# Kernel optimization log

Hardware: AMD Instinct MI355X
Metric: run time of the kernel (lower is better)

Reference implementation:

```python
import jax, jax.numpy as jnp
import numpy as np

KEY_DIM = 1024
SCALE = KEY_DIM ** -0.5


def setup_inputs() -> dict:
    key = jax.random.key(0)
    k1, k2, k3, k4 = jax.random.split(key, 4)
    B, S, E = 4, 2048, 1024
    x = jax.random.normal(k1, (B, S, E), dtype=jnp.float32)
    WQ = jax.random.normal(k2, (KEY_DIM, E), dtype=jnp.float32) * (E ** -0.5)
    WK = jax.random.normal(k3, (KEY_DIM, E), dtype=jnp.float32) * (E ** -0.5)
    WV = jax.random.normal(k4, (KEY_DIM, E), dtype=jnp.float32) * (E ** -0.5)
    return {"x": x, "WQ": WQ, "WK": WK, "WV": WV}


def reference(x, WQ, WK, WV):
    # x: [B, S, E]; Linear(bias=False) weights are [out, in] as in torch.
    q = jnp.einsum('bse,ke->bsk', x, WQ)   # [B, S, K]
    k = jnp.einsum('bse,ke->bsk', x, WK)   # [B, S, K]
    v = jnp.einsum('bse,ve->bsv', x, WV)   # [B, S, V]
    scores = jnp.einsum('bsk,btk->bst', q, k) * SCALE  # [B, S, S]
    # Faithful to torch: mask where tril(scores) == 0 (upper triangle).
    masked = jnp.where(jnp.tril(scores) == 0, -jnp.inf, scores)
    attn = jax.nn.softmax(masked, axis=-1)
    return jnp.einsum('bst,btv->bsv', attn, v)  # dropout=0.0 -> identity
```

## Files before the change

### kernel.cpp

```cpp
#include <hip/hip_runtime.h>

typedef _Float16 f16x8 __attribute__((ext_vector_type(8)));
typedef unsigned short u16x8v __attribute__((ext_vector_type(8)));
typedef unsigned short u16x4v __attribute__((ext_vector_type(4)));
typedef float f32x4 __attribute__((ext_vector_type(4)));

constexpr int SEQ = 2048;
constexpr int DIM = 1024;
constexpr int BATCH = 4;
constexpr size_t NBS = (size_t)BATCH * SEQ * DIM;

static __device__ __forceinline__ unsigned short f2h(float f) {
    return __builtin_bit_cast(unsigned short, (_Float16)f);
}
static __device__ __forceinline__ float h2f(unsigned short u) {
    return (float)__builtin_bit_cast(_Float16, u);
}
static __device__ __forceinline__ f16x8 ldsld(const unsigned short* p) {
    return __builtin_bit_cast(f16x8, *(const u16x8v*)p);
}
static __device__ __forceinline__ void gld_lds16(const unsigned short* g, unsigned short* l) {
    __builtin_amdgcn_global_load_lds(
        (const __attribute__((address_space(1))) void*)g,
        (__attribute__((address_space(3))) void*)l, 16, 0, 0);
}

__global__ __launch_bounds__(256) void cvt_all(
    const float* __restrict__ X,
    const float* __restrict__ W0, const float* __restrict__ W1,
    const float* __restrict__ W2,
    unsigned short* __restrict__ Xf, unsigned short* __restrict__ Wf)
{
    const int b = blockIdx.x;
    const float* src;
    unsigned short* dst;
    int i;
    if (b < 8192) {
        src = X; dst = Xf;
        i = b * 256 + threadIdx.x;
    } else {
        const int wb = b - 8192;
        const int z = wb >> 10;
        src = (z == 0) ? W0 : (z == 1) ? W1 : W2;
        dst = Wf + (size_t)z * DIM * DIM;
        i = (wb & 1023) * 256 + threadIdx.x;
    }
    float4 f = ((const float4*)src)[i];
    u16x4v h;
    h.x = f2h(f.x); h.y = f2h(f.y); h.z = f2h(f.z); h.w = f2h(f.w);
    ((u16x4v*)dst)[i] = h;
}

__global__ __launch_bounds__(256) void mt_gemm(
    const unsigned short* __restrict__ Wqf, const unsigned short* __restrict__ Wkf,
    unsigned short* __restrict__ Mt)
{
    __shared__ __attribute__((aligned(16))) unsigned short As[64 * 128];
    __shared__ __attribute__((aligned(16))) unsigned short Bs[64 * 128];
    const int e0p = blockIdx.x * 128;
    const int e0  = blockIdx.y * 128;
    const int tid = threadIdx.x;
    const int w = tid >> 6, lane = tid & 63, q = lane >> 4, c = lane & 15;
    const int wrow = (w >> 1) * 64, wcol = (w & 1) * 64;
    const int kr = lane >> 4;
    const int un = lane & 15;

    f32x4 acc[4][4];
#pragma unroll
    for (int a = 0; a < 4; ++a)
#pragma unroll
        for (int b = 0; b < 4; ++b) acc[a][b] = (f32x4){0.f, 0.f, 0.f, 0.f};

    for (int k0 = 0; k0 < DIM; k0 += 64) {
        __syncthreads();
#pragma unroll
        for (int j = 0; j < 4; ++j) {
            const size_t ga = (size_t)(k0 + w * 16 + j * 4 + kr) * DIM;
            unsigned short* la = As + (w * 16 + j * 4) * 128;
            unsigned short* lb = Bs + (w * 16 + j * 4) * 128;
            gld_lds16(Wkf + ga + e0p + un * 8, la);
            gld_lds16(Wqf + ga + e0  + un * 8, lb);
        }
        __syncthreads();
#pragma unroll
        for (int kk = 0; kk < 2; ++kk) {
            f16x8 af[4], bf[4];
#pragma unroll
            for (int mi = 0; mi < 4; ++mi) {
                u16x8v t_;
#pragma unroll
                for (int j = 0; j < 8; ++j)
                    t_[j] = As[(kk * 32 + q * 8 + j) * 128 + wrow + mi * 16 + c];
                af[mi] = __builtin_bit_cast(f16x8, t_);
            }
#pragma unroll
            for (int ni = 0; ni < 4; ++ni) {
                u16x8v t_;
#pragma unroll
                for (int j = 0; j < 8; ++j)
                    t_[j] = Bs[(kk * 32 + q * 8 + j) * 128 + wcol + ni * 16 + c];
                bf[ni] = __builtin_bit_cast(f16x8, t_);
            }
#pragma unroll
            for (int mi = 0; mi < 4; ++mi)
#pragma unroll
                for (int ni = 0; ni < 4; ++ni)
                    acc[mi][ni] = __builtin_amdgcn_mfma_f32_16x16x32_f16(af[mi], bf[ni], acc[mi][ni], 0, 0, 0);
        }
    }
#pragma unroll
    for (int mi = 0; mi < 4; ++mi)
#pragma unroll
        for (int ni = 0; ni < 4; ++ni) {
            const int col = e0 + wcol + ni * 16 + c;
#pragma unroll
            for (int r = 0; r < 4; ++r) {
                const int row = e0p + wrow + mi * 16 + q * 4 + r;
                Mt[(size_t)row * DIM + col] = f2h(acc[mi][ni][r]);
            }
        }
}

__global__ __launch_bounds__(256) void yv_gemm(
    const unsigned short* __restrict__ Xf, const unsigned short* __restrict__ Mt,
    const unsigned short* __restrict__ Wvf,
    unsigned short* __restrict__ Yf, unsigned short* __restrict__ Vt)
{
    __shared__ __attribute__((aligned(16))) unsigned short Ah[128 * 64];
    __shared__ __attribute__((aligned(16))) unsigned short Bh[128 * 64];
    const int m0 = blockIdx.x * 128, n0 = blockIdx.y * 128, z = blockIdx.z;
    const unsigned short* Wz = z ? Wvf : Mt;
    const int tid = threadIdx.x;
    const int w = tid >> 6, lane = tid & 63, q = lane >> 4, c = lane & 15;
    const int wrow = (w >> 1) * 64, wcol = (w & 1) * 64;
    const int g8 = lane >> 3;
    const int cu = (lane & 7) ^ g8;
    const int srow = w * 8 + g8;
    const int scol = cu * 8;
    unsigned short* lA = Ah + w * 512;
    unsigned short* lB = Bh + w * 512;
    const int c7 = c & 7;

    f32x4 acc[4][4];
#pragma unroll
    for (int a = 0; a < 4; ++a)
#pragma unroll
        for (int b = 0; b < 4; ++b) acc[a][b] = (f32x4){0.f, 0.f, 0.f, 0.f};

    for (int k0 = 0; k0 < DIM; k0 += 64) {
        __syncthreads();
        {
            const size_t ga = (size_t)(m0 + srow) * DIM + k0 + scol;
            const size_t gb = (size_t)(n0 + srow) * DIM + k0 + scol;
#pragma unroll
            for (int j = 0; j < 4; ++j) {
                gld_lds16(Xf + ga + (size_t)(j * 32) * DIM, lA + j * 2048);
                gld_lds16(Wz + gb + (size_t)(j * 32) * DIM, lB + j * 2048);
            }
        }
        __syncthreads();
#pragma unroll
        for (int kk = 0; kk < 2; ++kk) {
            f16x8 ah[4], bh[4];
#pragma unroll
            for (int mi = 0; mi < 4; ++mi)
                ah[mi] = ldsld(Ah + (wrow + mi * 16 + c) * 64 + (((kk << 2) + q) ^ c7) * 8);
#pragma unroll
            for (int ni = 0; ni < 4; ++ni)
                bh[ni] = ldsld(Bh + (wcol + ni * 16 + c) * 64 + (((kk << 2) + q) ^ c7) * 8);
#pragma unroll
            for (int mi = 0; mi < 4; ++mi)
#pragma unroll
                for (int ni = 0; ni < 4; ++ni)
                    acc[mi][ni] = __builtin_amdgcn_mfma_f32_16x16x32_f16(ah[mi], bh[ni], acc[mi][ni], 0, 0, 0);
        }
    }

    if (z == 1) {
#pragma unroll
        for (int mi = 0; mi < 4; ++mi) {
            const int mg = m0 + wrow + mi * 16 + q * 4;
            const int bb = mg >> 11, ss = mg & (SEQ - 1);
#pragma unroll
            for (int ni = 0; ni < 4; ++ni) {
                const int col = n0 + wcol + ni * 16 + c;
                u16x4v v;
                v.x = f2h(acc[mi][ni][0]);
                v.y = f2h(acc[mi][ni][1]);
                v.z = f2h(acc[mi][ni][2]);
                v.w = f2h(acc[mi][ni][3]);
                *(u16x4v*)(Vt + ((size_t)bb * DIM + col) * SEQ + ss) = v;
            }
        }
    } else {
#pragma unroll
        for (int mi = 0; mi < 4; ++mi)
#pragma unroll
            for (int ni = 0; ni < 4; ++ni) {
                const int col = n0 + wcol + ni * 16 + c;
#pragma unroll
                for (int r = 0; r < 4; ++r) {
                    const int row = m0 + wrow + mi * 16 + q * 4 + r;
                    Yf[(size_t)row * DIM + col] = f2h(acc[mi][ni][r]);
                }
            }
    }
}

__global__ __launch_bounds__(256) void scores_gemm1b(
    const unsigned short* __restrict__ Q, const unsigned short* __restrict__ K,
    unsigned short* __restrict__ S)
{
    __shared__ __attribute__((aligned(16))) unsigned short Ah[128 * 64];
    __shared__ __attribute__((aligned(16))) unsigned short Bh[128 * 64];
    const int t = blockIdx.x;
    int ti = (int)((__builtin_sqrtf(8.f * t + 1.f) - 1.f) * 0.5f);
    while ((ti + 1) * (ti + 2) / 2 <= t) ++ti;
    while (ti * (ti + 1) / 2 > t) --ti;
    const int tj = t - ti * (ti + 1) / 2;
    const int i0 = ti * 128, j0 = tj * 128, b = blockIdx.z;
    const unsigned short* Qb = Q + (size_t)b * SEQ * DIM;
    const unsigned short* Kb = K + (size_t)b * SEQ * DIM;
    unsigned short* Sb = S + (size_t)b * SEQ * SEQ;
    const int tid = threadIdx.x;
    const int w = tid >> 6, lane = tid & 63, q = lane >> 4, c = lane & 15;
    const int wrow = (w >> 1) * 64, wcol = (w & 1) * 64;
    const int g8 = lane >> 3;
    const int cu = (lane & 7) ^ g8;
    const int srow = w * 8 + g8;
    const int scol = cu * 8;
    unsigned short* lA = Ah + w * 512;
    unsigned short* lB = Bh + w * 512;
    const int c7 = c & 7;

    f32x4 acc[4][4];
#pragma unroll
    for (int a = 0; a < 4; ++a)
#pragma unroll
        for (int bq = 0; bq < 4; ++bq) acc[a][bq] = (f32x4){0.f, 0.f, 0.f, 0.f};

    for (int k0 = 0; k0 < DIM; k0 += 64) {
        __syncthreads();
        {
            const size_t ga = (size_t)(i0 + srow) * DIM + k0 + scol;
            const size_t gb = (size_t)(j0 + srow) * DIM + k0 + scol;
#pragma unroll
            for (int j = 0; j < 4; ++j) {
                gld_lds16(Qb + ga + (size_t)(j * 32) * DIM, lA + j * 2048);
                gld_lds16(Kb + gb + (size_t)(j * 32) * DIM, lB + j * 2048);
            }
        }
        __syncthreads();
#pragma unroll
        for (int kk = 0; kk < 2; ++kk) {
            f16x8 ah[4], bh[4];
#pragma unroll
            for (int mi = 0; mi < 4; ++mi)
                ah[mi] = ldsld(Ah + (wrow + mi * 16 + c) * 64 + (((kk << 2) + q) ^ c7) * 8);
#pragma unroll
            for (int ni = 0; ni < 4; ++ni)
                bh[ni] = ldsld(Bh + (wcol + ni * 16 + c) * 64 + (((kk << 2) + q) ^ c7) * 8);
#pragma unroll
            for (int mi = 0; mi < 4; ++mi)
#pragma unroll
                for (int ni = 0; ni < 4; ++ni)
                    acc[mi][ni] = __builtin_amdgcn_mfma_f32_16x16x32_f16(ah[mi], bh[ni], acc[mi][ni], 0, 0, 0);
        }
    }
#pragma unroll
    for (int mi = 0; mi < 4; ++mi)
#pragma unroll
        for (int ni = 0; ni < 4; ++ni) {
            const int col = j0 + wcol + ni * 16 + c;
#pragma unroll
            for (int r = 0; r < 4; ++r) {
                const int row = i0 + wrow + mi * 16 + q * 4 + r;
                const float sc = acc[mi][ni][r] * 0.03125f;
                Sb[(size_t)row * SEQ + col] =
                    (sc == 0.f) ? (unsigned short)0xFC00u : f2h(sc);
            }
        }
}

__global__ __launch_bounds__(256) void softmax_row_b(
    const unsigned short* __restrict__ S, unsigned short* __restrict__ P)
{
    const int i = blockIdx.x, t = threadIdx.x;
    const size_t ro = ((size_t)blockIdx.y * SEQ + i) * SEQ;
    const int wid = t >> 6, lane = t & 63;
    __shared__ float redm[4], reds[4];
    const int j0 = t * 8;
    const int rti = (i & ~127) + 128;
    float sv[8];
    float mx = -__builtin_inff();
    if (j0 <= i) {
        u16x8v raw = *(const u16x8v*)(S + ro + j0);
#pragma unroll
        for (int u = 0; u < 8; ++u) {
            float s = (j0 + u <= i) ? h2f(raw[u]) : -__builtin_inff();
            sv[u] = s;
            mx = fmaxf(mx, s);
        }
    } else {
#pragma unroll
        for (int u = 0; u < 8; ++u) sv[u] = -__builtin_inff();
    }
#pragma unroll
    for (int off = 1; off < 64; off <<= 1) mx = fmaxf(mx, __shfl_xor(mx, off));
    if (lane == 0) redm[wid] = mx;
    __syncthreads();
    const float M = fmaxf(fmaxf(redm[0], redm[1]), fmaxf(redm[2], redm[3]));
    float sum = 0.f;
#pragma unroll
    for (int u = 0; u < 8; ++u) {
        float e = __expf(sv[u] - M);
        sv[u] = e;
        sum += e;
    }
#pragma unroll
    for (int off = 1; off < 64; off <<= 1) sum += __shfl_xor(sum, off);
    if (lane == 0) reds[wid] = sum;
    __syncthreads();
    const float rinv = 1.f / (reds[0] + reds[1] + reds[2] + reds[3]);
    if (j0 < rti) {
        u16x8v o;
#pragma unroll
        for (int u = 0; u < 8; ++u) o[u] = f2h(sv[u] * rinv);
        *(u16x8v*)(P + ro + j0) = o;
    }
}

__global__ __launch_bounds__(256) void pv_gemm(
    const unsigned short* __restrict__ Pm, const unsigned short* __restrict__ Vt,
    float* __restrict__ Out)
{
    __shared__ __attribute__((aligned(16))) unsigned short Ps[128 * 64];
    __shared__ __attribute__((aligned(16))) unsigned short Vs[128 * 64];
    const int b = blockIdx.z;
    const int i0t = (b < 2) ? blockIdx.x : 15 - blockIdx.x;
    const int i0 = i0t * 128, d0 = blockIdx.y * 128;
    const int tid = threadIdx.x;
    const int w = tid >> 6, lane = tid & 63, q = lane >> 4, c = lane & 15;
    const int wrow = (w >> 1) * 64, wcol = (w & 1) * 64;
    const int g8 = lane >> 3;
    const int cu = (lane & 7) ^ g8;
    const int srow = w * 8 + g8;
    const int scol = cu * 8;
    unsigned short* lA = Ps + w * 512;
    unsigned short* lB = Vs + w * 512;
    const int c7 = c & 7;

    f32x4 acc[4][4];
#pragma unroll
    for (int a = 0; a < 4; ++a)
#pragma unroll
        for (int bq = 0; bq < 4; ++bq) acc[a][bq] = (f32x4){0.f, 0.f, 0.f, 0.f};

    const int njs = 2 * i0t + 2;

    for (int ks = 0; ks < njs; ++ks) {
        const int j0 = ks * 64;
        __syncthreads();
        {
            const size_t gpa = ((size_t)b * SEQ + i0 + srow) * SEQ + j0 + scol;
            const size_t gva = ((size_t)b * DIM + d0 + srow) * SEQ + j0 + scol;
#pragma unroll
            for (int j = 0; j < 4; ++j) {
                gld_lds16(Pm + gpa + (size_t)(j * 32) * SEQ, lA + j * 2048);
                gld_lds16(Vt + gva + (size_t)(j * 32) * SEQ, lB + j * 2048);
            }
        }
        __syncthreads();
#pragma unroll
        for (int kk = 0; kk < 2; ++kk) {
            f16x8 ah[4], bh[4];
#pragma unroll
            for (int mi = 0; mi < 4; ++mi)
                ah[mi] = ldsld(Ps + (wrow + mi * 16 + c) * 64 + (((kk << 2) + q) ^ c7) * 8);
#pragma unroll
            for (int ni = 0; ni < 4; ++ni)
                bh[ni] = ldsld(Vs + (wcol + ni * 16 + c) * 64 + (((kk << 2) + q) ^ c7) * 8);
#pragma unroll
            for (int mi = 0; mi < 4; ++mi)
#pragma unroll
                for (int ni = 0; ni < 4; ++ni)
                    acc[mi][ni] = __builtin_amdgcn_mfma_f32_16x16x32_f16(ah[mi], bh[ni], acc[mi][ni], 0, 0, 0);
        }
    }
#pragma unroll
    for (int mi = 0; mi < 4; ++mi)
#pragma unroll
        for (int ni = 0; ni < 4; ++ni) {
            const int dcol = d0 + wcol + ni * 16 + c;
#pragma unroll
            for (int r = 0; r < 4; ++r) {
                const int i = i0 + wrow + mi * 16 + q * 4 + r;
                Out[((size_t)b * SEQ + i) * DIM + dcol] = acc[mi][ni][r];
            }
        }
}

extern "C" void kernel_launch(void* const* d_in, const int* in_sizes, int n_in,
                              void* d_out, int out_size, void* d_ws, size_t ws_size,
                              hipStream_t stream)
{
    (void)out_size; (void)ws_size;
    const float* X = nullptr;
    const float* Wv[3] = {nullptr, nullptr, nullptr};
    int nw = 0;
    for (int i = 0; i < n_in; ++i) {
        if (in_sizes[i] == (int)NBS)
            X = (const float*)d_in[i];
        else if (nw < 3)
            Wv[nw++] = (const float*)d_in[i];
    }

    unsigned short* ws = (unsigned short*)d_ws;
    unsigned short* Yf = ws;
    unsigned short* Vt = ws + 2 * NBS;
    unsigned short* Xf = ws + 3 * NBS;
    unsigned short* Pp = ws + 3 * NBS;
    unsigned short* Sb = ws + 5 * NBS;
    unsigned short* Wf = ws + 7 * NBS;
    unsigned short* Mtb = Wf + (size_t)3 * DIM * DIM;
    float* Out = (float*)d_out;

    cvt_all<<<dim3(8192 + 3072), 256, 0, stream>>>(X, Wv[0], Wv[1], Wv[2], Xf, Wf);

    mt_gemm<<<dim3(8, 8), 256, 0, stream>>>(
        Wf, Wf + (size_t)DIM * DIM, Mtb);

    yv_gemm<<<dim3(64, 8, 2), 256, 0, stream>>>(
        Xf, Mtb, Wf + (size_t)2 * DIM * DIM, Yf, Vt);

    scores_gemm1b<<<dim3(136, 1, BATCH), 256, 0, stream>>>(Yf, Xf, Sb);
    softmax_row_b<<<dim3(SEQ, BATCH), 256, 0, stream>>>(Sb, Pp);

    pv_gemm<<<dim3(16, 8, BATCH), 256, 0, stream>>>(Pp, Vt, Out);
}
```

Baseline: 259.1 us.

## Pre-transpose WQ/WK in convert kernel, swizzle mt_gemm LDS, remap scores grid

```diff
diff --git a/kernel.cpp b/kernel.cpp
--- a/kernel.cpp
+++ b/kernel.cpp
@@ -29,78 +29,103 @@
     const float* __restrict__ X,
     const float* __restrict__ W0, const float* __restrict__ W1,
     const float* __restrict__ W2,
-    unsigned short* __restrict__ Xf, unsigned short* __restrict__ Wf)
-{
+    unsigned short* __restrict__ Xf, unsigned short* __restrict__ Wf,
+    unsigned short* __restrict__ WqT, unsigned short* __restrict__ WkT)
+{
+    __shared__ __attribute__((aligned(16))) unsigned short T[64][72];
     const int b = blockIdx.x;
-    const float* src;
-    unsigned short* dst;
-    int i;
-    if (b < 8192) {
-        src = X; dst = Xf;
-        i = b * 256 + threadIdx.x;
-    } else {
-        const int wb = b - 8192;
-        const int z = wb >> 10;
-        src = (z == 0) ? W0 : (z == 1) ? W1 : W2;
-        dst = Wf + (size_t)z * DIM * DIM;
-        i = (wb & 1023) * 256 + threadIdx.x;
-    }
-    float4 f = ((const float4*)src)[i];
-    u16x4v h;
-    h.x = f2h(f.x); h.y = f2h(f.y); h.z = f2h(f.z); h.w = f2h(f.w);
-    ((u16x4v*)dst)[i] = h;
+    const int t = threadIdx.x;
+    if (b < 11264) {
+        const float* src;
+        unsigned short* dst;
+        int i;
+        if (b < 8192) {
+            src = X; dst = Xf;
+            i = b * 256 + t;
+        } else {
+            const int wb = b - 8192;
+            const int z = wb >> 10;
+            src = (z == 0) ? W0 : (z == 1) ? W1 : W2;
+            dst = Wf + (size_t)z * DIM * DIM;
+            i = (wb & 1023) * 256 + t;
+        }
+        float4 f = ((const float4*)src)[i];
+        u16x4v h;
+        h.x = f2h(f.x); h.y = f2h(f.y); h.z = f2h(f.z); h.w = f2h(f.w);
+        ((u16x4v*)dst)[i] = h;
+        return;
+    }
+    const int tb = b - 11264;
+    const float* src = (tb < 256) ? W0 : W1;
+    unsigned short* dst = (tb < 256) ? WqT : WkT;
+    const int tile = tb & 255;
+    const int tk = (tile >> 4) * 64;
+    const int te = (tile & 15) * 64;
+    const int cu = t & 15, kr4 = t >> 4;
+#pragma unroll
+    for (int p = 0; p < 4; ++p) {
+        const int k = p * 16 + kr4;
+        float4 v = *(const float4*)(src + (size_t)(tk + k) * DIM + te + cu * 4);
+        T[cu * 4 + 0][k] = f2h(v.x);
+        T[cu * 4 + 1][k] = f2h(v.y);
+        T[cu * 4 + 2][k] = f2h(v.z);
+        T[cu * 4 + 3][k] = f2h(v.w);
+    }
+    __syncthreads();
+    const int un = t & 7, er = t >> 3;
+#pragma unroll
+    for (int p = 0; p < 2; ++p) {
+        const int e = p * 32 + er;
+        *(u16x8v*)(dst + (size_t)(te + e) * DIM + tk + un * 8) =
+            *(const u16x8v*)&T[e][un * 8];
+    }
 }
 
 __global__ __launch_bounds__(256) void mt_gemm(
-    const unsigned short* __restrict__ Wqf, const unsigned short* __restrict__ Wkf,
+    const unsigned short* __restrict__ WkTp, const unsigned short* __restrict__ WqTp,
     unsigned short* __restrict__ Mt)
 {
-    __shared__ __attribute__((aligned(16))) unsigned short As[64 * 128];
-    __shared__ __attribute__((aligned(16))) unsigned short Bs[64 * 128];
-    const int e0p = blockIdx.x * 128;
-    const int e0  = blockIdx.y * 128;
+    __shared__ __attribute__((aligned(16))) unsigned short Ah[128 * 64];
+    __shared__ __attribute__((aligned(16))) unsigned short Bh[128 * 64];
+    const int m0 = blockIdx.x * 128, n0 = blockIdx.y * 128;
     const int tid = threadIdx.x;
     const int w = tid >> 6, lane = tid & 63, q = lane >> 4, c = lane & 15;
     const int wrow = (w >> 1) * 64, wcol = (w & 1) * 64;
-    const int kr = lane >> 4;
-    const int un = lane & 15;
+    const int g8 = lane >> 3;
+    const int cu = (lane & 7) ^ g8;
+    const int srow = w * 8 + g8;
+    const int scol = cu * 8;
+    unsigned short* lA = Ah + w * 512;
+    unsigned short* lB = Bh + w * 512;
+    const int c7 = c & 7;
 
     f32x4 acc[4][4];
 #pragma unroll
     for (int a = 0; a < 4; ++a)
 #pragma unroll
-        for (int b = 0; b < 4; ++b) acc[a][b] = (f32x4){0.f, 0.f, 0.f, 0.f};
+        for (int bq = 0; bq < 4; ++bq) acc[a][bq] = (f32x4){0.f, 0.f, 0.f, 0.f};
 
     for (int k0 = 0; k0 < DIM; k0 += 64) {
         __syncthreads();
-#pragma unroll
-        for (int j = 0; j < 4; ++j) {
-            const size_t ga = (size_t)(k0 + w * 16 + j * 4 + kr) * DIM;
-            unsigned short* la = As + (w * 16 + j * 4) * 128;
-            unsigned short* lb = Bs + (w * 16 + j * 4) * 128;
-            gld_lds16(Wkf + ga + e0p + un * 8, la);
-            gld_lds16(Wqf + ga + e0  + un * 8, lb);
+        {
+            const size_t ga = (size_t)(m0 + srow) * DIM + k0 + scol;
+            const size_t gb = (size_t)(n0 + srow) * DIM + k0 + scol;
+#pragma unroll
+            for (int j = 0; j < 4; ++j) {
+                gld_lds16(WkTp + ga + (size_t)(j * 32) * DIM, lA + j * 2048);
+                gld_lds16(WqTp + gb + (size_t)(j * 32) * DIM, lB + j * 2048);
+            }
         }
         __syncthreads();
 #pragma unroll
         for (int kk = 0; kk < 2; ++kk) {
             f16x8 af[4], bf[4];
 #pragma unroll
-            for (int mi = 0; mi < 4; ++mi) {
-                u16x8v t_;
-#pragma unroll
-                for (int j = 0; j < 8; ++j)
-                    t_[j] = As[(kk * 32 + q * 8 + j) * 128 + wrow + mi * 16 + c];
-                af[mi] = __builtin_bit_cast(f16x8, t_);
-            }
-#pragma unroll
-            for (int ni = 0; ni < 4; ++ni) {
-                u16x8v t_;
-#pragma unroll
-                for (int j = 0; j < 8; ++j)
-                    t_[j] = Bs[(kk * 32 + q * 8 + j) * 128 + wcol + ni * 16 + c];
-                bf[ni] = __builtin_bit_cast(f16x8, t_);
-            }
+            for (int mi = 0; mi < 4; ++mi)
+                af[mi] = ldsld(Ah + (wrow + mi * 16 + c) * 64 + (((kk << 2) + q) ^ c7) * 8);
+#pragma unroll
+            for (int ni = 0; ni < 4; ++ni)
+                bf[ni] = ldsld(Bh + (wcol + ni * 16 + c) * 64 + (((kk << 2) + q) ^ c7) * 8);
 #pragma unroll
             for (int mi = 0; mi < 4; ++mi)
 #pragma unroll
@@ -112,10 +137,10 @@
     for (int mi = 0; mi < 4; ++mi)
 #pragma unroll
         for (int ni = 0; ni < 4; ++ni) {
-            const int col = e0 + wcol + ni * 16 + c;
+            const int col = n0 + wcol + ni * 16 + c;
 #pragma unroll
             for (int r = 0; r < 4; ++r) {
-                const int row = e0p + wrow + mi * 16 + q * 4 + r;
+                const int row = m0 + wrow + mi * 16 + q * 4 + r;
                 Mt[(size_t)row * DIM + col] = f2h(acc[mi][ni][r]);
             }
         }
@@ -213,12 +238,15 @@
 {
     __shared__ __attribute__((aligned(16))) unsigned short Ah[128 * 64];
     __shared__ __attribute__((aligned(16))) unsigned short Bh[128 * 64];
-    const int t = blockIdx.x;
+    const int flat = blockIdx.x;
+    const int wg = (flat & 7) * 68 + (flat >> 3);
+    const int b = wg / 136;
+    const int t = wg - b * 136;
     int ti = (int)((__builtin_sqrtf(8.f * t + 1.f) - 1.f) * 0.5f);
     while ((ti + 1) * (ti + 2) / 2 <= t) ++ti;
     while (ti * (ti + 1) / 2 > t) --ti;
     const int tj = t - ti * (ti + 1) / 2;
-    const int i0 = ti * 128, j0 = tj * 128, b = blockIdx.z;
+    const int i0 = ti * 128, j0 = tj * 128;
     const unsigned short* Qb = Q + (size_t)b * SEQ * DIM;
     const unsigned short* Kb = K + (size_t)b * SEQ * DIM;
     unsigned short* Sb = S + (size_t)b * SEQ * SEQ;
@@ -423,17 +451,19 @@
     unsigned short* Sb = ws + 5 * NBS;
     unsigned short* Wf = ws + 7 * NBS;
     unsigned short* Mtb = Wf + (size_t)3 * DIM * DIM;
+    unsigned short* WqT = Mtb + (size_t)DIM * DIM;
+    unsigned short* WkT = WqT + (size_t)DIM * DIM;
     float* Out = (float*)d_out;
 
-    cvt_all<<<dim3(8192 + 3072), 256, 0, stream>>>(X, Wv[0], Wv[1], Wv[2], Xf, Wf);
-
-    mt_gemm<<<dim3(8, 8), 256, 0, stream>>>(
-        Wf, Wf + (size_t)DIM * DIM, Mtb);
+    cvt_all<<<dim3(8192 + 3072 + 512), 256, 0, stream>>>(
+        X, Wv[0], Wv[1], Wv[2], Xf, Wf, WqT, WkT);
+
+    mt_gemm<<<dim3(8, 8), 256, 0, stream>>>(WkT, WqT, Mtb);
 
     yv_gemm<<<dim3(64, 8, 2), 256, 0, stream>>>(
         Xf, Mtb, Wf + (size_t)2 * DIM * DIM, Yf, Vt);
 
-    scores_gemm1b<<<dim3(136, 1, BATCH), 256, 0, stream>>>(Yf, Xf, Sb);
+    scores_gemm1b<<<dim3(544), 256, 0, stream>>>(Yf, Xf, Sb);
     softmax_row_b<<<dim3(SEQ, BATCH), 256, 0, stream>>>(Sb, Pp);
 
     pv_gemm<<<dim3(16, 8, BATCH), 256, 0, stream>>>(Pp, Vt, Out);
```

After: 237.2 us. 1.09x faster.
